# Kernel tuning notes

Hardware: AMD Instinct MI355X
Metric: run time of the kernel (lower is better)

## Reference

```python
import jax, jax.numpy as jnp
import numpy as np

EMB = 1024
HEADS = 16
HEAD_DIM = EMB // HEADS  # 64


def setup_inputs() -> dict:
    key = jax.random.key(0)
    ks = jax.random.split(key, 11)
    B, S = 2, 2048
    scale = 1.0 / np.sqrt(EMB)
    inp = {
        "xv": jax.random.normal(ks[0], (B, S, EMB), jnp.float32),
        "xk": jax.random.normal(ks[1], (B, S, EMB), jnp.float32),
        "xq": jax.random.normal(ks[2], (B, S, EMB), jnp.float32),
        "Wq": jax.random.normal(ks[3], (EMB, EMB), jnp.float32) * scale,
        "bq": jax.random.normal(ks[4], (EMB,), jnp.float32) * 0.01,
        "Wk": jax.random.normal(ks[5], (EMB, EMB), jnp.float32) * scale,
        "bk": jax.random.normal(ks[6], (EMB,), jnp.float32) * 0.01,
        "Wv": jax.random.normal(ks[7], (EMB, EMB), jnp.float32) * scale,
        "bv": jax.random.normal(ks[8], (EMB,), jnp.float32) * 0.01,
        "Wo": jax.random.normal(ks[9], (EMB, EMB), jnp.float32) * scale,
        "bo": jax.random.normal(ks[10], (EMB,), jnp.float32) * 0.01,
    }
    return inp


def reference(xv, xk, xq, Wq, bq, Wk, bk, Wv, bv, Wo, bo):
    B, S, E = xq.shape
    H, D = HEADS, HEAD_DIM
    # projections (x @ W + b), split into heads: [B,S,H,D]
    Q = (xq @ Wq + bq).reshape(B, S, H, D)
    K = (xk @ Wk + bk).reshape(B, S, H, D)
    V = (xv @ Wv + bv).reshape(B, S, H, D)
    # scaled dot-product attention per head (vectorized over heads)
    scores = jnp.einsum("bqhd,bkhd->bhqk", Q, K) / jnp.sqrt(jnp.float32(D))
    attn = jax.nn.softmax(scores, axis=-1)
    ctx = jnp.einsum("bhqk,bkhd->bqhd", attn, V).reshape(B, S, E)
    return ctx @ Wo + bo
```

## Files before the change

### kernel.cpp

```cpp
#include <hip/hip_runtime.h>
#include <hip/hip_bf16.h>

typedef __hip_bfloat16 bf16;
typedef __attribute__((ext_vector_type(8))) short short8;
typedef __attribute__((ext_vector_type(4))) short short4v;
typedef __attribute__((ext_vector_type(4))) float floatx4;

#define MFMA16 __builtin_amdgcn_mfma_f32_16x16x32_bf16


__device__ __forceinline__ void gl16(const void* g, void* l) {
    __builtin_amdgcn_global_load_lds(
        (const __attribute__((address_space(1))) void*)g,
        (__attribute__((address_space(3))) void*)l, 16, 0, 0);
}

__global__ __launch_bounds__(256) void wtrans_k(const float* __restrict__ w0,
                                                const float* __restrict__ w1,
                                                const float* __restrict__ w2,
                                                const float* __restrict__ w3,
                                                bf16* __restrict__ dst) {
    const float* srcs[4] = {w0, w1, w2, w3};
    const float* src = srcs[blockIdx.z];
    bf16* d = dst + (size_t)blockIdx.z * 1024 * 1024;
    __shared__ float t[32][33];
    int tx = threadIdx.x, ty = threadIdx.y;
    int x0 = blockIdx.x * 32, y0 = blockIdx.y * 32;
#pragma unroll
    for (int i = 0; i < 4; i++)
        t[ty + i * 8][tx] = src[(size_t)(y0 + ty + i * 8) * 1024 + x0 + tx];
    __syncthreads();
#pragma unroll
    for (int i = 0; i < 4; i++)
        d[(size_t)(x0 + ty + i * 8) * 1024 + y0 + tx] =
            __float2bfloat16(t[tx][ty + i * 8]);
}

__global__ __launch_bounds__(256) void qkv_k(const float* __restrict__ xq,
                                             const float* __restrict__ xk,
                                             const float* __restrict__ xv,
                                             const bf16* __restrict__ wt,
                                             const float* __restrict__ bq,
                                             const float* __restrict__ bk,
                                             const float* __restrict__ bv,
                                             bf16* __restrict__ Qw,
                                             bf16* __restrict__ Kw,
                                             bf16* __restrict__ Vt) {
    __shared__ __align__(16) float lAf[128 * 32];
    __shared__ __align__(16) bf16 lB[128 * 32];
    int z = blockIdx.z;
    const float* A = (z == 0) ? xq : (z == 1) ? xk : xv;
    const bf16* Bt = wt + (size_t)z * (1024 * 1024);
    const float* bias = (z == 0) ? bq : (z == 1) ? bk : bv;
    int m0 = blockIdx.x * 128, n0 = blockIdx.y * 128;
    int tid = threadIdx.x, wave = tid >> 6, lane = tid & 63;
    int lm = lane & 15, quad = lane >> 4;
    int wm = wave >> 1, wn = wave & 1;
    int s7 = lm & 7;
    int swb = quad ^ ((lm >> 1) & 3);

    floatx4 acc[4][4];
#pragma unroll
    for (int i = 0; i < 4; i++)
#pragma unroll
        for (int j = 0; j < 4; j++) acc[i][j] = (floatx4){0.f, 0.f, 0.f, 0.f};

    for (int kt = 0; kt < 32; kt++) {
#pragma unroll
        for (int q2 = 0; q2 < 4; q2++) {
            int slot0 = wave * 256 + q2 * 64;
            int r = (slot0 + lane) >> 3;
            int c = (lane & 7) ^ (r & 7);
            gl16(&A[(size_t)(m0 + r) * 1024 + kt * 32 + c * 4], &lAf[slot0 * 4]);
        }
#pragma unroll
        for (int q2 = 0; q2 < 2; q2++) {
            int slot0 = wave * 128 + q2 * 64;
            int r = (slot0 + lane) >> 2;
            int c = (lane & 3) ^ ((r >> 1) & 3);
            gl16(&Bt[(size_t)(n0 + r) * 1024 + kt * 32 + c * 8], &lB[slot0 * 8]);
        }
        __syncthreads();

        short8 af[4], bfr[4];
#pragma unroll
        for (int ms = 0; ms < 4; ms++) {
            int r = wm * 64 + ms * 16 + lm;
            float4 a0 = *(const float4*)&lAf[(r * 8 + ((2 * quad) ^ s7)) * 4];
            float4 a1 = *(const float4*)&lAf[(r * 8 + ((2 * quad + 1) ^ s7)) * 4];
            union { __hip_bfloat162 h2[4]; short8 s; } pk;
            pk.h2[0] = __float22bfloat162_rn(make_float2(a0.x, a0.y));
            pk.h2[1] = __float22bfloat162_rn(make_float2(a0.z, a0.w));
            pk.h2[2] = __float22bfloat162_rn(make_float2(a1.x, a1.y));
            pk.h2[3] = __float22bfloat162_rn(make_float2(a1.z, a1.w));
            af[ms] = pk.s;
        }
#pragma unroll
        for (int ns = 0; ns < 4; ns++) {
            int r = wn * 64 + ns * 16 + lm;
            bfr[ns] = *(const short8*)&lB[(r * 4 + swb) * 8];
        }
#pragma unroll
        for (int ms = 0; ms < 4; ms++)
#pragma unroll
            for (int ns = 0; ns < 4; ns++)
                acc[ms][ns] = MFMA16(af[ms], bfr[ns], acc[ms][ns], 0, 0, 0);
        __syncthreads();
    }

    bf16* dstQK = (z == 0) ? Qw : Kw;
    float scale = (z == 0) ? 0.125f : 1.0f;
#pragma unroll
    for (int ms = 0; ms < 4; ms++) {
        int rowb = m0 + wm * 64 + ms * 16 + quad * 4;
        int bb = rowb >> 11, s0 = rowb & 2047;
#pragma unroll
        for (int ns = 0; ns < 4; ns++) {
            int col = n0 + wn * 64 + ns * 16 + lm;
            float bvv = bias[col];
            int hh = col >> 6, d = col & 63;
            if (z < 2) {
#pragma unroll
                for (int rr = 0; rr < 4; rr++) {
                    float v = (acc[ms][ns][rr] + bvv) * scale;
                    dstQK[((((size_t)bb * 16 + hh) * 2048 + s0 + rr) << 6) + d] =
                        __float2bfloat16(v);
                }
            } else {
                short4v pk;
#pragma unroll
                for (int rr = 0; rr < 4; rr++) {
                    bf16 h = __float2bfloat16(acc[ms][ns][rr] + bvv);
                    pk[rr] = *(short*)&h;
                }
                *(short4v*)&Vt[((((size_t)bb * 16 + hh) * 64 + d) << 11) + s0] = pk;
            }
        }
    }
}

__global__ __launch_bounds__(256) void outproj_k(const bf16* __restrict__ ctx,
                                                 const bf16* __restrict__ wot,
                                                 const float* __restrict__ bo,
                                                 float* __restrict__ out) {
    __shared__ __align__(16) bf16 lA[128 * 32];
    __shared__ __align__(16) bf16 lB[64 * 32];
    int m0 = blockIdx.x * 128, n0 = blockIdx.y * 64;
    int tid = threadIdx.x, wave = tid >> 6, lane = tid & 63;
    int lm = lane & 15, quad = lane >> 4;
    int wm = wave >> 1, wn = wave & 1;
    int swb = quad ^ ((lm >> 1) & 3);

    floatx4 acc[4][2];
#pragma unroll
    for (int i = 0; i < 4; i++)
#pragma unroll
        for (int j = 0; j < 2; j++) acc[i][j] = (floatx4){0.f, 0.f, 0.f, 0.f};

    for (int kt = 0; kt < 32; kt++) {
#pragma unroll
        for (int q2 = 0; q2 < 2; q2++) {
            int slot0 = wave * 128 + q2 * 64;
            int r = (slot0 + lane) >> 2;
            int c = (lane & 3) ^ ((r >> 1) & 3);
            gl16(&ctx[(size_t)(m0 + r) * 1024 + kt * 32 + c * 8], &lA[slot0 * 8]);
        }
        {
            int slot0 = wave * 64;
            int r = (slot0 + lane) >> 2;
            int c = (lane & 3) ^ ((r >> 1) & 3);
            gl16(&wot[(size_t)(n0 + r) * 1024 + kt * 32 + c * 8], &lB[slot0 * 8]);
        }
        __syncthreads();

        short8 af[4], bfr[2];
#pragma unroll
        for (int ms = 0; ms < 4; ms++) {
            int r = wm * 64 + ms * 16 + lm;
            af[ms] = *(const short8*)&lA[(r * 4 + swb) * 8];
        }
#pragma unroll
        for (int ns = 0; ns < 2; ns++) {
            int r = wn * 32 + ns * 16 + lm;
            bfr[ns] = *(const short8*)&lB[(r * 4 + swb) * 8];
        }
#pragma unroll
        for (int ms = 0; ms < 4; ms++)
#pragma unroll
            for (int ns = 0; ns < 2; ns++)
                acc[ms][ns] = MFMA16(af[ms], bfr[ns], acc[ms][ns], 0, 0, 0);
        __syncthreads();
    }

#pragma unroll
    for (int ms = 0; ms < 4; ms++) {
        int rowb = m0 + wm * 64 + ms * 16 + quad * 4;
#pragma unroll
        for (int ns = 0; ns < 2; ns++) {
            int col = n0 + wn * 32 + ns * 16 + lm;
            float bvv = bo[col];
#pragma unroll
            for (int rr = 0; rr < 4; rr++)
                out[(size_t)(rowb + rr) * 1024 + col] = acc[ms][ns][rr] + bvv;
        }
    }
}

__global__ __launch_bounds__(256) void attn_k(const bf16* __restrict__ Q,
                                              const bf16* __restrict__ K,
                                              const bf16* __restrict__ Vt,
                                              bf16* __restrict__ ctx) {
    __shared__ __align__(16) bf16 lK[64 * 64];
    __shared__ __align__(16) bf16 lV[64 * 64];
    __shared__ __align__(16) bf16 lP[64 * 72];
    int bh = blockIdx.x, qt = blockIdx.y;
    int b = bh >> 4, h = bh & 15;
    const bf16* Qh = Q + (size_t)bh * (2048 * 64);
    const bf16* Kh = K + (size_t)bh * (2048 * 64);
    const bf16* Vh = Vt + (size_t)bh * (64 * 2048);
    int tid = threadIdx.x, wave = tid >> 6, lane = tid & 63;
    int lm = lane & 15, quad = lane >> 4;
    int s7 = lm & 7;

    int qrow = qt * 64 + wave * 16 + lm;
    short8 qf0 = *(const short8*)&Qh[(size_t)qrow * 64 + quad * 8];
    short8 qf1 = *(const short8*)&Qh[(size_t)qrow * 64 + 32 + quad * 8];

    floatx4 o[4];
#pragma unroll
    for (int i = 0; i < 4; i++) o[i] = (floatx4){0.f, 0.f, 0.f, 0.f};
    float lpart[4] = {0.f, 0.f, 0.f, 0.f};

    for (int kt = 0; kt < 32; kt++) {
#pragma unroll
        for (int q2 = 0; q2 < 2; q2++) {
            int slot0 = wave * 128 + q2 * 64;
            int r = (slot0 + lane) >> 3;
            int c = (lane & 7) ^ (r & 7);
            gl16(&Kh[(size_t)(kt * 64 + r) * 64 + c * 8], &lK[slot0 * 8]);
            gl16(&Vh[(size_t)r * 2048 + kt * 64 + c * 8], &lV[slot0 * 8]);
        }
        __syncthreads();

        floatx4 s[4];
#pragma unroll
        for (int i = 0; i < 4; i++) s[i] = (floatx4){0.f, 0.f, 0.f, 0.f};
#pragma unroll
        for (int ns = 0; ns < 4; ns++) {
            int r = ns * 16 + lm;
            short8 kf0 = *(const short8*)&lK[(r * 8 + (quad ^ s7)) * 8];
            short8 kf1 = *(const short8*)&lK[(r * 8 + ((4 + quad) ^ s7)) * 8];
            s[ns] = MFMA16(qf0, kf0, s[ns], 0, 0, 0);
            s[ns] = MFMA16(qf1, kf1, s[ns], 0, 0, 0);
        }

#pragma unroll
        for (int rr = 0; rr < 4; rr++) {
            float p0 = __expf(s[0][rr]);
            float p1 = __expf(s[1][rr]);
            float p2 = __expf(s[2][rr]);
            float p3 = __expf(s[3][rr]);
            lpart[rr] += (p0 + p1) + (p2 + p3);
            int row = (wave * 16 + quad * 4 + rr) * 72;
            lP[row + lm] = __float2bfloat16(p0);
            lP[row + 16 + lm] = __float2bfloat16(p1);
            lP[row + 32 + lm] = __float2bfloat16(p2);
            lP[row + 48 + lm] = __float2bfloat16(p3);
        }

#pragma unroll
        for (int kk = 0; kk < 2; kk++) {
            short8 pf = *(const short8*)&lP[(wave * 16 + lm) * 72 + kk * 32 + quad * 8];
#pragma unroll
            for (int ns = 0; ns < 4; ns++) {
                int r = ns * 16 + lm;
                short8 vf = *(const short8*)&lV[(r * 8 + ((kk * 4 + quad) ^ s7)) * 8];
                o[ns] = MFMA16(pf, vf, o[ns], 0, 0, 0);
            }
        }
        __syncthreads();
    }

    float inv[4];
#pragma unroll
    for (int rr = 0; rr < 4; rr++) {
        float l = lpart[rr];
        l += __shfl_xor(l, 1, 64);
        l += __shfl_xor(l, 2, 64);
        l += __shfl_xor(l, 4, 64);
        l += __shfl_xor(l, 8, 64);
        inv[rr] = 1.f / l;
    }

#pragma unroll
    for (int ns = 0; ns < 4; ns++) {
        int e = h * 64 + ns * 16 + lm;
#pragma unroll
        for (int rr = 0; rr < 4; rr++) {
            int srow = qt * 64 + wave * 16 + quad * 4 + rr;
            ctx[(size_t)(b * 2048 + srow) * 1024 + e] =
                __float2bfloat16(o[ns][rr] * inv[rr]);
        }
    }
}

extern "C" void kernel_launch(void* const* d_in, const int* in_sizes, int n_in,
                              void* d_out, int out_size, void* d_ws, size_t ws_size,
                              hipStream_t stream) {
    const float* xv = (const float*)d_in[0];
    const float* xk = (const float*)d_in[1];
    const float* xq = (const float*)d_in[2];
    const float* Wq = (const float*)d_in[3];
    const float* bq = (const float*)d_in[4];
    const float* Wk = (const float*)d_in[5];
    const float* bk = (const float*)d_in[6];
    const float* Wv = (const float*)d_in[7];
    const float* bv = (const float*)d_in[8];
    const float* Wo = (const float*)d_in[9];
    const float* bo = (const float*)d_in[10];
    float* out = (float*)d_out;
    bf16* ws = (bf16*)d_ws;

    const size_t MB1 = 1024 * 1024;
    bf16* wt  = ws;
    bf16* Qw  = ws + 4 * MB1;
    bf16* Kw  = ws + 8 * MB1;
    bf16* Vt  = ws + 12 * MB1;
    bf16* ctx = ws + 16 * MB1;

    hipLaunchKernelGGL(wtrans_k, dim3(32, 32, 4), dim3(32, 8), 0, stream,
                       Wq, Wk, Wv, Wo, wt);

    hipLaunchKernelGGL(qkv_k, dim3(32, 8, 3), dim3(256), 0, stream,
                       xq, xk, xv, wt, bq, bk, bv, Qw, Kw, Vt);

    hipLaunchKernelGGL(attn_k, dim3(32, 32), dim3(256), 0, stream, Qw, Kw, Vt, ctx);

    hipLaunchKernelGGL(outproj_k, dim3(32, 16), dim3(256), 0, stream,
                       ctx, wt + 3 * MB1, bo, out);
}
```

Measured before the change: 245.4 us.

## Double-buffer LDS tiles in all GEMM/attention kernels and use exp2 softmax

Adds two LDS buffers to the QKV projection, output projection and attention kernels, so the next tile's global-to-LDS load is issued before the current tile is computed. The goal is to hide global load latency behind the MFMA work. It also folds log2(e) into the Q scale so the softmax can use the hardware exp2 instead of __expf. The extra LDS per block may lower occupancy, and the prefetch relies on the single end-of-iteration barrier to order buffer reuse.

Measured after the change: 266.9 us. 8.7% more time.

```diff
diff --git a/kernel.cpp b/kernel.cpp
--- a/kernel.cpp
+++ b/kernel.cpp
@@ -46,8 +46,8 @@
                                              bf16* __restrict__ Qw,
                                              bf16* __restrict__ Kw,
                                              bf16* __restrict__ Vt) {
-    __shared__ __align__(16) float lAf[128 * 32];
-    __shared__ __align__(16) bf16 lB[128 * 32];
+    __shared__ __align__(16) float lAf[2][128 * 32];
+    __shared__ __align__(16) bf16 lB[2][128 * 32];
     int z = blockIdx.z;
     const float* A = (z == 0) ? xq : (z == 1) ? xk : xv;
     const bf16* Bt = wt + (size_t)z * (1024 * 1024);
@@ -65,29 +65,36 @@
 #pragma unroll
         for (int j = 0; j < 4; j++) acc[i][j] = (floatx4){0.f, 0.f, 0.f, 0.f};
 
-    for (int kt = 0; kt < 32; kt++) {
+    auto stage = [&](int kt, int bi) {
 #pragma unroll
         for (int q2 = 0; q2 < 4; q2++) {
             int slot0 = wave * 256 + q2 * 64;
             int r = (slot0 + lane) >> 3;
             int c = (lane & 7) ^ (r & 7);
-            gl16(&A[(size_t)(m0 + r) * 1024 + kt * 32 + c * 4], &lAf[slot0 * 4]);
+            gl16(&A[(size_t)(m0 + r) * 1024 + kt * 32 + c * 4], &lAf[bi][slot0 * 4]);
         }
 #pragma unroll
         for (int q2 = 0; q2 < 2; q2++) {
             int slot0 = wave * 128 + q2 * 64;
             int r = (slot0 + lane) >> 2;
             int c = (lane & 3) ^ ((r >> 1) & 3);
-            gl16(&Bt[(size_t)(n0 + r) * 1024 + kt * 32 + c * 8], &lB[slot0 * 8]);
-        }
-        __syncthreads();
+            gl16(&Bt[(size_t)(n0 + r) * 1024 + kt * 32 + c * 8], &lB[bi][slot0 * 8]);
+        }
+    };
+
+    stage(0, 0);
+    __syncthreads();
+
+    for (int kt = 0; kt < 32; kt++) {
+        int cur = kt & 1;
+        if (kt + 1 < 32) stage(kt + 1, cur ^ 1);
 
         short8 af[4], bfr[4];
 #pragma unroll
         for (int ms = 0; ms < 4; ms++) {
             int r = wm * 64 + ms * 16 + lm;
-            float4 a0 = *(const float4*)&lAf[(r * 8 + ((2 * quad) ^ s7)) * 4];
-            float4 a1 = *(const float4*)&lAf[(r * 8 + ((2 * quad + 1) ^ s7)) * 4];
+            float4 a0 = *(const float4*)&lAf[cur][(r * 8 + ((2 * quad) ^ s7)) * 4];
+            float4 a1 = *(const float4*)&lAf[cur][(r * 8 + ((2 * quad + 1) ^ s7)) * 4];
             union { __hip_bfloat162 h2[4]; short8 s; } pk;
             pk.h2[0] = __float22bfloat162_rn(make_float2(a0.x, a0.y));
             pk.h2[1] = __float22bfloat162_rn(make_float2(a0.z, a0.w));
@@ -98,7 +105,7 @@
 #pragma unroll
         for (int ns = 0; ns < 4; ns++) {
             int r = wn * 64 + ns * 16 + lm;
-            bfr[ns] = *(const short8*)&lB[(r * 4 + swb) * 8];
+            bfr[ns] = *(const short8*)&lB[cur][(r * 4 + swb) * 8];
         }
 #pragma unroll
         for (int ms = 0; ms < 4; ms++)
@@ -109,7 +116,8 @@
     }
 
     bf16* dstQK = (z == 0) ? Qw : Kw;
-    float scale = (z == 0) ? 0.125f : 1.0f;
+    const float QSCALE = 0.18033688011112042f;
+    float scale = (z == 0) ? QSCALE : 1.0f;
 #pragma unroll
     for (int ms = 0; ms < 4; ms++) {
         int rowb = m0 + wm * 64 + ms * 16 + quad * 4;
@@ -143,8 +151,8 @@
                                                  const bf16* __restrict__ wot,
                                                  const float* __restrict__ bo,
                                                  float* __restrict__ out) {
-    __shared__ __align__(16) bf16 lA[128 * 32];
-    __shared__ __align__(16) bf16 lB[64 * 32];
+    __shared__ __align__(16) bf16 lA[2][128 * 32];
+    __shared__ __align__(16) bf16 lB[2][64 * 32];
     int m0 = blockIdx.x * 128, n0 = blockIdx.y * 64;
     int tid = threadIdx.x, wave = tid >> 6, lane = tid & 63;
     int lm = lane & 15, quad = lane >> 4;
@@ -157,32 +165,39 @@
 #pragma unroll
         for (int j = 0; j < 2; j++) acc[i][j] = (floatx4){0.f, 0.f, 0.f, 0.f};
 
-    for (int kt = 0; kt < 32; kt++) {
+    auto stage = [&](int kt, int bi) {
 #pragma unroll
         for (int q2 = 0; q2 < 2; q2++) {
             int slot0 = wave * 128 + q2 * 64;
             int r = (slot0 + lane) >> 2;
             int c = (lane & 3) ^ ((r >> 1) & 3);
-            gl16(&ctx[(size_t)(m0 + r) * 1024 + kt * 32 + c * 8], &lA[slot0 * 8]);
+            gl16(&ctx[(size_t)(m0 + r) * 1024 + kt * 32 + c * 8], &lA[bi][slot0 * 8]);
         }
         {
             int slot0 = wave * 64;
             int r = (slot0 + lane) >> 2;
             int c = (lane & 3) ^ ((r >> 1) & 3);
-            gl16(&wot[(size_t)(n0 + r) * 1024 + kt * 32 + c * 8], &lB[slot0 * 8]);
-        }
-        __syncthreads();
+            gl16(&wot[(size_t)(n0 + r) * 1024 + kt * 32 + c * 8], &lB[bi][slot0 * 8]);
+        }
+    };
+
+    stage(0, 0);
+    __syncthreads();
+
+    for (int kt = 0; kt < 32; kt++) {
+        int cur = kt & 1;
+        if (kt + 1 < 32) stage(kt + 1, cur ^ 1);
 
         short8 af[4], bfr[2];
 #pragma unroll
         for (int ms = 0; ms < 4; ms++) {
             int r = wm * 64 + ms * 16 + lm;
-            af[ms] = *(const short8*)&lA[(r * 4 + swb) * 8];
+            af[ms] = *(const short8*)&lA[cur][(r * 4 + swb) * 8];
         }
 #pragma unroll
         for (int ns = 0; ns < 2; ns++) {
             int r = wn * 32 + ns * 16 + lm;
-            bfr[ns] = *(const short8*)&lB[(r * 4 + swb) * 8];
+            bfr[ns] = *(const short8*)&lB[cur][(r * 4 + swb) * 8];
         }
 #pragma unroll
         for (int ms = 0; ms < 4; ms++)
@@ -210,8 +225,8 @@
                                               const bf16* __restrict__ K,
                                               const bf16* __restrict__ Vt,
                                               bf16* __restrict__ ctx) {
-    __shared__ __align__(16) bf16 lK[64 * 64];
-    __shared__ __align__(16) bf16 lV[64 * 64];
+    __shared__ __align__(16) bf16 lK[2][64 * 64];
+    __shared__ __align__(16) bf16 lV[2][64 * 64];
     __shared__ __align__(16) bf16 lP[64 * 72];
     int bh = blockIdx.x, qt = blockIdx.y;
     int b = bh >> 4, h = bh & 15;
@@ -231,16 +246,23 @@
     for (int i = 0; i < 4; i++) o[i] = (floatx4){0.f, 0.f, 0.f, 0.f};
     float lpart[4] = {0.f, 0.f, 0.f, 0.f};
 
-    for (int kt = 0; kt < 32; kt++) {
+    auto stage = [&](int kt, int bi) {
 #pragma unroll
         for (int q2 = 0; q2 < 2; q2++) {
             int slot0 = wave * 128 + q2 * 64;
             int r = (slot0 + lane) >> 3;
             int c = (lane & 7) ^ (r & 7);
-            gl16(&Kh[(size_t)(kt * 64 + r) * 64 + c * 8], &lK[slot0 * 8]);
-            gl16(&Vh[(size_t)r * 2048 + kt * 64 + c * 8], &lV[slot0 * 8]);
-        }
-        __syncthreads();
+            gl16(&Kh[(size_t)(kt * 64 + r) * 64 + c * 8], &lK[bi][slot0 * 8]);
+            gl16(&Vh[(size_t)r * 2048 + kt * 64 + c * 8], &lV[bi][slot0 * 8]);
+        }
+    };
+
+    stage(0, 0);
+    __syncthreads();
+
+    for (int kt = 0; kt < 32; kt++) {
+        int cur = kt & 1;
+        if (kt + 1 < 32) stage(kt + 1, cur ^ 1);
 
         floatx4 s[4];
 #pragma unroll
@@ -248,18 +270,18 @@
 #pragma unroll
         for (int ns = 0; ns < 4; ns++) {
             int r = ns * 16 + lm;
-            short8 kf0 = *(const short8*)&lK[(r * 8 + (quad ^ s7)) * 8];
-            short8 kf1 = *(const short8*)&lK[(r * 8 + ((4 + quad) ^ s7)) * 8];
+            short8 kf0 = *(const short8*)&lK[cur][(r * 8 + (quad ^ s7)) * 8];
+            short8 kf1 = *(const short8*)&lK[cur][(r * 8 + ((4 + quad) ^ s7)) * 8];
             s[ns] = MFMA16(qf0, kf0, s[ns], 0, 0, 0);
             s[ns] = MFMA16(qf1, kf1, s[ns], 0, 0, 0);
         }
 
 #pragma unroll
         for (int rr = 0; rr < 4; rr++) {
-            float p0 = __expf(s[0][rr]);
-            float p1 = __expf(s[1][rr]);
-            float p2 = __expf(s[2][rr]);
-            float p3 = __expf(s[3][rr]);
+            float p0 = __builtin_amdgcn_exp2f(s[0][rr]);
+            float p1 = __builtin_amdgcn_exp2f(s[1][rr]);
+            float p2 = __builtin_amdgcn_exp2f(s[2][rr]);
+            float p3 = __builtin_amdgcn_exp2f(s[3][rr]);
             lpart[rr] += (p0 + p1) + (p2 + p3);
             int row = (wave * 16 + quad * 4 + rr) * 72;
             lP[row + lm] = __float2bfloat16(p0);
@@ -274,7 +296,7 @@
 #pragma unroll
             for (int ns = 0; ns < 4; ns++) {
                 int r = ns * 16 + lm;
-                short8 vf = *(const short8*)&lV[(r * 8 + ((kk * 4 + quad) ^ s7)) * 8];
+                short8 vf = *(const short8*)&lV[cur][(r * 8 + ((kk * 4 + quad) ^ s7)) * 8];
                 o[ns] = MFMA16(pf, vf, o[ns], 0, 0, 0);
             }
         }
```
